# Optimization experiments

Hardware: AMD Instinct MI355X
Metric: run time of the kernel (lower is better)

## Reference

```python
import jax, jax.numpy as jnp
import numpy as np

NA = 100000   # author nodes
NP = 100000   # paper nodes
E = 500000    # edges per relation
H = 128       # hidden size
FA = 256      # author input features
FP = 128      # paper input features
LA = 4        # author labels
LP = 7        # paper labels


def setup_inputs() -> dict:
    key = jax.random.key(0)
    ks = iter(jax.random.split(key, 48))
    def rn(shape, scale=0.05):
        return jax.random.normal(next(ks), shape, jnp.float32) * scale
    inp = {}
    inp['x_author'] = jax.random.normal(next(ks), (NA, FA), jnp.float32)
    inp['x_paper'] = jax.random.normal(next(ks), (NP, FP), jnp.float32)
    inp['edge_index_p2a'] = jax.random.randint(next(ks), (2, E), 0, 100000, jnp.int64)  # row0: paper src, row1: author dst
    inp['edge_index_a2p'] = jax.random.randint(next(ks), (2, E), 0, 100000, jnp.int64)  # row0: author src, row1: paper dst
    # layer 1 convs (per message type): lin_src, lin_dst, lin_update(2H->H)
    inp['w1_p2a_src'] = rn((FP, H)); inp['b1_p2a_src'] = rn((H,))
    inp['w1_p2a_dst'] = rn((FA, H)); inp['b1_p2a_dst'] = rn((H,))
    inp['w1_p2a_upd'] = rn((2 * H, H)); inp['b1_p2a_upd'] = rn((H,))
    inp['w1_a2p_src'] = rn((FA, H)); inp['b1_a2p_src'] = rn((H,))
    inp['w1_a2p_dst'] = rn((FP, H)); inp['b1_a2p_dst'] = rn((H,))
    inp['w1_a2p_upd'] = rn((2 * H, H)); inp['b1_a2p_upd'] = rn((H,))
    # layer 2 convs (all dims = H)
    inp['w2_p2a_src'] = rn((H, H)); inp['b2_p2a_src'] = rn((H,))
    inp['w2_p2a_dst'] = rn((H, H)); inp['b2_p2a_dst'] = rn((H,))
    inp['w2_p2a_upd'] = rn((2 * H, H)); inp['b2_p2a_upd'] = rn((H,))
    inp['w2_a2p_src'] = rn((H, H)); inp['b2_a2p_src'] = rn((H,))
    inp['w2_a2p_dst'] = rn((H, H)); inp['b2_a2p_dst'] = rn((H,))
    inp['w2_a2p_upd'] = rn((2 * H, H)); inp['b2_a2p_upd'] = rn((H,))
    # batchnorm affine params per node type per layer
    inp['g1_a'] = jnp.ones((H,), jnp.float32); inp['be1_a'] = jnp.zeros((H,), jnp.float32)
    inp['g1_p'] = jnp.ones((H,), jnp.float32); inp['be1_p'] = jnp.zeros((H,), jnp.float32)
    inp['g2_a'] = jnp.ones((H,), jnp.float32); inp['be2_a'] = jnp.zeros((H,), jnp.float32)
    inp['g2_p'] = jnp.ones((H,), jnp.float32); inp['be2_p'] = jnp.zeros((H,), jnp.float32)
    # post message-passing heads
    inp['w_post_a'] = rn((H, LA)); inp['b_post_a'] = rn((LA,))
    inp['w_post_p'] = rn((H, LP)); inp['b_post_p'] = rn((LP,))
    return inp


def _mean_agg(x_src, src, dst, n_dst):
    # gather source features along edges, mean-scatter to destination nodes
    msg = x_src[src]                                            # [E, F]
    s = jax.ops.segment_sum(msg, dst, num_segments=n_dst)       # [n_dst, F]
    cnt = jax.ops.segment_sum(jnp.ones((dst.shape[0],), msg.dtype), dst, num_segments=n_dst)
    return s / jnp.maximum(cnt, 1.0)[:, None]


def _conv(x_src, x_dst, src, dst, ws, bs, wd, bd, wu, bu):
    agg = _mean_agg(x_src, src, dst, x_dst.shape[0])
    h = jnp.concatenate([x_dst @ wd + bd, agg @ ws + bs], axis=-1)   # [n_dst, 2H]
    return h @ wu + bu


def _bn_lrelu(x, g, b):
    # BatchNorm1d(eps=1) in training mode (batch stats, biased var) then LeakyReLU(0.01)
    m = x.mean(axis=0)
    v = x.var(axis=0)
    y = g * (x - m) / jnp.sqrt(v + 1.0) + b
    return jnp.where(y >= 0, y, 0.01 * y)


def reference(x_author, x_paper, edge_index_p2a, edge_index_a2p,
              w1_p2a_src, b1_p2a_src, w1_p2a_dst, b1_p2a_dst, w1_p2a_upd, b1_p2a_upd,
              w1_a2p_src, b1_a2p_src, w1_a2p_dst, b1_a2p_dst, w1_a2p_upd, b1_a2p_upd,
              w2_p2a_src, b2_p2a_src, w2_p2a_dst, b2_p2a_dst, w2_p2a_upd, b2_p2a_upd,
              w2_a2p_src, b2_a2p_src, w2_a2p_dst, b2_a2p_dst, w2_a2p_upd, b2_a2p_upd,
              g1_a, be1_a, g1_p, be1_p, g2_a, be2_a, g2_p, be2_p,
              w_post_a, b_post_a, w_post_p, b_post_p):
    src_pa, dst_pa = edge_index_p2a[0], edge_index_p2a[1]
    src_ap, dst_ap = edge_index_a2p[0], edge_index_a2p[1]
    # layer 1: per-message-type conv -> per-node-type BN + LeakyReLU
    h_a = _conv(x_paper, x_author, src_pa, dst_pa, w1_p2a_src, b1_p2a_src, w1_p2a_dst, b1_p2a_dst, w1_p2a_upd, b1_p2a_upd)
    h_p = _conv(x_author, x_paper, src_ap, dst_ap, w1_a2p_src, b1_a2p_src, w1_a2p_dst, b1_a2p_dst, w1_a2p_upd, b1_a2p_upd)
    h_a = _bn_lrelu(h_a, g1_a, be1_a)
    h_p = _bn_lrelu(h_p, g1_p, be1_p)
    # layer 2
    h_a2 = _conv(h_p, h_a, src_pa, dst_pa, w2_p2a_src, b2_p2a_src, w2_p2a_dst, b2_p2a_dst, w2_p2a_upd, b2_p2a_upd)
    h_p2 = _conv(h_a, h_p, src_ap, dst_ap, w2_a2p_src, b2_a2p_src, w2_a2p_dst, b2_a2p_dst, w2_a2p_upd, b2_a2p_upd)
    h_a2 = _bn_lrelu(h_a2, g2_a, be2_a)
    h_p2 = _bn_lrelu(h_p2, g2_p, be2_p)
    # post message-passing heads per node type
    out_a = h_a2 @ w_post_a + b_post_a   # [NA, LA]
    out_p = h_p2 @ w_post_p + b_post_p   # [NP, LP]
    return (out_a, out_p)
```

## Files before the change

kernel.cpp:

```cpp
#include <hip/hip_runtime.h>

#define NN 100000
#define NE 500000
#define HD 128
#define NBLK 391

typedef float f32x4v __attribute__((ext_vector_type(4)));
typedef short s16x8  __attribute__((ext_vector_type(8)));

static __device__ __forceinline__ unsigned f2bf_bits(float f){
  unsigned u = __float_as_uint(f);
  return (u + 0x7FFF + ((u >> 16) & 1)) >> 16;
}
static __device__ __forceinline__ void split8v(f32x4v v0, f32x4v v1, s16x8& hi, s16x8& lo){
  #pragma unroll
  for (int j = 0; j < 4; ++j){
    float f = v0[j];
    unsigned hb = f2bf_bits(f);
    hi[j] = (short)hb; lo[j] = (short)f2bf_bits(f - __uint_as_float(hb << 16));
  }
  #pragma unroll
  for (int j = 0; j < 4; ++j){
    float f = v1[j];
    unsigned hb = f2bf_bits(f);
    hi[4+j] = (short)hb; lo[4+j] = (short)f2bf_bits(f - __uint_as_float(hb << 16));
  }
}

static __device__ __forceinline__ float4 bn_lrelu4(float4 v, float4 sc, float4 sh){
  v.x = v.x*sc.x + sh.x; v.x = v.x >= 0.f ? v.x : 0.01f*v.x;
  v.y = v.y*sc.y + sh.y; v.y = v.y >= 0.f ? v.y : 0.01f*v.y;
  v.z = v.z*sc.z + sh.z; v.z = v.z >= 0.f ? v.z : 0.01f*v.z;
  v.w = v.w*sc.w + sh.w; v.w = v.w >= 0.f ? v.w : 0.01f*v.w;
  return v;
}
static __device__ __forceinline__ f32x4v bn_lrelu4v(f32x4v v, f32x4v sc, f32x4v sh){
  #pragma unroll
  for (int j = 0; j < 4; ++j){
    float y = v[j]*sc[j] + sh[j];
    v[j] = y >= 0.f ? y : 0.01f*y;
  }
  return v;
}

__global__ void k_count(const int* __restrict__ ei_pa, const int* __restrict__ ei_ap,
                        int* __restrict__ deg2){
  int idx = blockIdx.x * 256 + threadIdx.x;
  if (idx < NE)        atomicAdd(&deg2[      ei_pa[NE + idx]], 1);
  else if (idx < 2*NE) atomicAdd(&deg2[NN + ei_ap[NE + (idx - NE)]], 1);
}

__global__ void k_bsum(const int* __restrict__ deg2, int* __restrict__ bsum){
  int rel = blockIdx.x / NBLK, b = blockIdx.x % NBLK;
  int i = b*256 + threadIdx.x;
  int v = (i < NN) ? deg2[rel*NN + i] : 0;
  __shared__ int s[256];
  s[threadIdx.x] = v; __syncthreads();
  for (int o = 128; o > 0; o >>= 1){
    if (threadIdx.x < o) s[threadIdx.x] += s[threadIdx.x + o];
    __syncthreads();
  }
  if (threadIdx.x == 0) bsum[rel*512 + b] = s[0];
}

__global__ void k_bscan(const int* __restrict__ bsum, int* __restrict__ bsoff){
  int rel = blockIdx.x, t = threadIdx.x;
  int v = (t < NBLK) ? bsum[rel*512 + t] : 0;
  __shared__ int s[512];
  s[t] = v; __syncthreads();
  for (int o = 1; o < 512; o <<= 1){
    int x = (t >= o) ? s[t - o] : 0;
    __syncthreads();
    s[t] += x;
    __syncthreads();
  }
  bsoff[rel*512 + t] = s[t] - v;
}

__global__ void k_scanC(const int* __restrict__ deg2, const int* __restrict__ bsoff,
                        int* __restrict__ off2, int* __restrict__ cur2){
  int rel = blockIdx.x / NBLK, b = blockIdx.x % NBLK;
  int i = b*256 + threadIdx.x, t = threadIdx.x;
  int v = (i < NN) ? deg2[rel*NN + i] : 0;
  __shared__ int s[256];
  s[t] = v; __syncthreads();
  for (int o = 1; o < 256; o <<= 1){
    int x = (t >= o) ? s[t - o] : 0;
    __syncthreads();
    s[t] += x;
    __syncthreads();
  }
  if (i < NN){
    int o = bsoff[rel*512 + b] + s[t] - v;
    off2[rel*NN + i] = o;
    cur2[rel*NN + i] = o;
  }
}

__global__ void k_fill(const int* __restrict__ ei_pa, const int* __restrict__ ei_ap,
                       int* __restrict__ cur2,
                       int* __restrict__ col_pa, int* __restrict__ col_ap){
  int idx = blockIdx.x * 256 + threadIdx.x;
  if (idx < NE){
    int s = ei_pa[idx], d = ei_pa[NE + idx];
    int pos = atomicAdd(&cur2[d], 1);
    col_pa[pos] = s;
  } else if (idx < 2*NE){
    int e = idx - NE;
    int s = ei_ap[e], d = ei_ap[NE + e];
    int pos = atomicAdd(&cur2[NN + d], 1);
    col_ap[pos] = s;
  }
}

struct FoldDesc { const float* A; const float* B; short* T; int off; };
struct FoldArgs { FoldDesc d[8]; int rs[9]; };

__global__ void k_fold(FoldArgs fa){
  int row = blockIdx.x;
  int seg = 0;
  #pragma unroll
  for (int s = 0; s < 8; ++s) if (row >= fa.rs[s+1]) seg = s + 1;
  int m = row - fa.rs[seg];
  const float* A = fa.d[seg].A + (size_t)m * 128;
  const float* B = fa.d[seg].B;
  int n = threadIdx.x;
  float acc = 0.f;
  for (int k = 0; k < 128; ++k) acc += A[k] * B[k*128 + n];
  unsigned hb = f2bf_bits(acc);
  float hf = __uint_as_float(hb << 16);
  unsigned lb = f2bf_bits(acc - hf);
  int gkc = fa.d[seg].off + (m >> 5), quad = (m >> 3) & 3, j = m & 7;
  int lane = quad*16 + (n & 15), nt = n >> 4;
  size_t fb = (size_t)((gkc*8 + nt)*2)*512 + lane*8 + j;
  fa.d[seg].T[fb]       = (short)hb;
  fa.d[seg].T[fb + 512] = (short)lb;
}

struct BiasArgs { const float* bd[4]; const float* bs[4]; const float* wu[4];
                  const float* bu[4]; float* outb[4]; };
__global__ void k_biasfold(BiasArgs ba){
  int s = blockIdx.x, j = threadIdx.x;
  const float* wu = ba.wu[s];
  float acc = ba.bu[s][j];
  for (int k = 0; k < 128; ++k)
    acc += ba.bd[s][k] * wu[k*128 + j] + ba.bs[s][k] * wu[(128 + k)*128 + j];
  ba.outb[s][j] = acc;
}

template<int DUALB, int GATHER, int BN>
__global__ __launch_bounds__(256)
void k_gemm3(const float* __restrict__ A1, int lda1, int KC1,
             const float* __restrict__ bn1,
             const float* __restrict__ A2, int lda2, int KC2,
             const short* __restrict__ BfA, const short* __restrict__ BfB,
             const float* __restrict__ bias,
             const int* __restrict__ goff, const int* __restrict__ gdeg,
             const int* __restrict__ gcol, const float* __restrict__ gsrc,
             float* __restrict__ C1, float* __restrict__ C2,
             float* __restrict__ stats, int M)
{
  constexpr int BUFSZ = DUALB ? 32768 : 16384;
  constexpr int LDSSZ = 2*BUFSZ + (BN ? 1024 : 0);
  __shared__ __align__(16) char smem[LDSSZ];
  float* bnlds = (float*)(smem + 2*BUFSZ);

  const int tid  = threadIdx.x;
  const int wave = tid >> 6, lane = tid & 63;
  const int li   = lane & 15, quad = lane >> 4;
  const int rowT = blockIdx.x * 128 + wave * 32;
  const int KCtot = KC1 + KC2;

  f32x4v acc1[2][8];
  f32x4v acc2[2][8];
  #pragma unroll
  for (int mt = 0; mt < 2; ++mt)
    #pragma unroll
    for (int nt = 0; nt < 8; ++nt){
      acc1[mt][nt] = (f32x4v){0.f, 0.f, 0.f, 0.f};
      if (DUALB) acc2[mt][nt] = (f32x4v){0.f, 0.f, 0.f, 0.f};
    }

  const float* b1[2];
  const float* b2[2];
  #pragma unroll
  for (int mt = 0; mt < 2; ++mt){
    int row = rowT + mt*16 + li;
    int r = (row < M) ? row : 0;
    b1[mt] = A1 + (size_t)r*lda1 + quad*8;
    b2[mt] = A2 ? (A2 + (size_t)r*lda2 + quad*8) : (const float*)nullptr;
  }

  auto loadA = [&](int gkc, f32x4v (&dst)[2][2]){
    #pragma unroll
    for (int mt = 0; mt < 2; ++mt){
      const float* p = (gkc < KC1) ? (b1[mt] + gkc*32) : (b2[mt] + (gkc - KC1)*32);
      dst[mt][0] = *(const f32x4v*)p;
      dst[mt][1] = *(const f32x4v*)(p + 4);
    }
  };

  auto stageB = [&](int kc, int bufIdx){
    char* d = smem + bufIdx * BUFSZ;
    const char* sA = (const char*)BfA + (size_t)kc * 16384;
    #pragma unroll
    for (int c = 0; c < 4; ++c){
      int off = c*4096 + wave*1024;
      __builtin_amdgcn_global_load_lds(
          (const __attribute__((address_space(1))) unsigned int*)(sA + off + lane*16),
          (__attribute__((address_space(3))) unsigned int*)(d + off),
          16, 0, 0);
    }
    if (DUALB && kc < KC1){
      const char* sB = (const char*)BfB + (size_t)kc * 16384;
      #pragma unroll
      for (int c = 0; c < 4; ++c){
        int off = c*4096 + wave*1024;
        __builtin_amdgcn_global_load_lds(
            (const __attribute__((address_space(1))) unsigned int*)(sB + off + lane*16),
            (__attribute__((address_space(3))) unsigned int*)(d + 16384 + off),
            16, 0, 0);
      }
    }
  };

  auto computeK = [&](int j, int bufIdx, f32x4v (&a)[2][2]){
    if (BN && j < KC1){
      int base = j*32 + quad*8;
      f32x4v sc0 = *(const f32x4v*)(bnlds + base);
      f32x4v sc1 = *(const f32x4v*)(bnlds + base + 4);
      f32x4v sh0 = *(const f32x4v*)(bnlds + base + 128);
      f32x4v sh1 = *(const f32x4v*)(bnlds + base + 132);
      #pragma unroll
      for (int mt = 0; mt < 2; ++mt){
        a[mt][0] = bn_lrelu4v(a[mt][0], sc0, sh0);
        a[mt][1] = bn_lrelu4v(a[mt][1], sc1, sh1);
      }
    }
    s16x8 ah[2], al[2];
    #pragma unroll
    for (int mt = 0; mt < 2; ++mt) split8v(a[mt][0], a[mt][1], ah[mt], al[mt]);

    const short* base = (const short*)(smem + bufIdx*BUFSZ) + lane*8;
    __builtin_amdgcn_s_setprio(1);
    #pragma unroll
    for (int nt = 0; nt < 8; ++nt){
      const short* bp = base + (nt << 10);
      s16x8 bh = *(const s16x8*)bp;
      s16x8 bl = *(const s16x8*)(bp + 512);
      #pragma unroll
      for (int mt = 0; mt < 2; ++mt){
        acc1[mt][nt] = __builtin_amdgcn_mfma_f32_16x16x32_bf16(ah[mt], bh, acc1[mt][nt], 0, 0, 0);
        acc1[mt][nt] = __builtin_amdgcn_mfma_f32_16x16x32_bf16(al[mt], bh, acc1[mt][nt], 0, 0, 0);
        acc1[mt][nt] = __builtin_amdgcn_mfma_f32_16x16x32_bf16(ah[mt], bl, acc1[mt][nt], 0, 0, 0);
      }
    }
    if (DUALB && j < KC1){
      const short* base2 = base + 8192;
      #pragma unroll
      for (int nt = 0; nt < 8; ++nt){
        const short* bp = base2 + (nt << 10);
        s16x8 bh = *(const s16x8*)bp;
        s16x8 bl = *(const s16x8*)(bp + 512);
        #pragma unroll
        for (int mt = 0; mt < 2; ++mt){
          acc2[mt][nt] = __builtin_amdgcn_mfma_f32_16x16x32_bf16(ah[mt], bh, acc2[mt][nt], 0, 0, 0);
          acc2[mt][nt] = __builtin_amdgcn_mfma_f32_16x16x32_bf16(al[mt], bh, acc2[mt][nt], 0, 0, 0);
          acc2[mt][nt] = __builtin_amdgcn_mfma_f32_16x16x32_bf16(ah[mt], bl, acc2[mt][nt], 0, 0, 0);
        }
      }
    }
    __builtin_amdgcn_s_setprio(0);
  };

  if (BN) bnlds[tid] = bn1[tid];
  f32x4v aC[2][2], aN1[2][2], aN2[2][2];
  stageB(0, 0);
  loadA(0, aC);
  loadA(1, aN1);
  if (BN) asm volatile("s_waitcnt lgkmcnt(0)" ::: "memory");

  for (int j = 0; j < KCtot; ++j){
    if (j + 1 < KCtot) asm volatile("s_waitcnt vmcnt(4)" ::: "memory");
    else               asm volatile("s_waitcnt vmcnt(0)" ::: "memory");
    __builtin_amdgcn_s_barrier();
    __builtin_amdgcn_sched_barrier(0);
    if (j + 1 < KCtot) stageB(j + 1, (j + 1) & 1);
    if (j + 2 < KCtot) loadA(j + 2, aN2);
    computeK(j, j & 1, aC);
    #pragma unroll
    for (int mt = 0; mt < 2; ++mt){
      aC[mt][0] = aN1[mt][0]; aC[mt][1] = aN1[mt][1];
      aN1[mt][0] = aN2[mt][0]; aN1[mt][1] = aN2[mt][1];
    }
  }

  __syncthreads();
  float* Cw = (float*)smem + wave*2048;
  int col4 = lane & 31;
  float4 s1 = make_float4(0.f,0.f,0.f,0.f), s2 = s1;

  auto epi_pass = [&](f32x4v (&ac)[2][8], float* Cout, const float* bptr,
                      bool wStats){
    float4 bias4 = make_float4(0.f,0.f,0.f,0.f);
    if (bptr) bias4 = ((const float4*)bptr)[col4];
    #pragma unroll
    for (int mt = 0; mt < 2; ++mt){
      #pragma unroll
      for (int r = 0; r < 4; ++r){
        int lr = quad*4 + r;
        #pragma unroll
        for (int nt = 0; nt < 8; ++nt){
          int c = nt*16 + li;
          int chunk = ((c >> 2) + 2*quad) & 31;
          Cw[lr*128 + chunk*4 + (c & 3)] = ac[mt][nt][r];
        }
      }
      #pragma unroll
      for (int i = 0; i < 8; ++i){
        int lr = i*2 + (lane >> 5);
        int grow = rowT + mt*16 + lr;
        if (grow >= M) continue;
        int chunk = (col4 + 2*(lr >> 2)) & 31;
        float4 v = *(const float4*)(Cw + lr*128 + chunk*4);
        v.x += bias4.x; v.y += bias4.y; v.z += bias4.z; v.w += bias4.w;
        if (GATHER && wStats){
          int cnt = gdeg[grow], s0g = goff[grow];
          float4 g = make_float4(0.f,0.f,0.f,0.f);
          for (int e = 0; e < cnt; ++e){
            int src = gcol[s0g + e];
            float4 gv = ((const float4*)(gsrc + ((size_t)src << 7)))[col4];
            g.x += gv.x; g.y += gv.y; g.z += gv.z; g.w += gv.w;
          }
          float inv = 1.0f / (float)(cnt > 0 ? cnt : 1);
          v.x += g.x*inv; v.y += g.y*inv; v.z += g.z*inv; v.w += g.w*inv;
        }
        ((float4*)(Cout + ((size_t)grow << 7)))[col4] = v;
        if (wStats){
          s1.x += v.x; s1.y += v.y; s1.z += v.z; s1.w += v.w;
          s2.x += v.x*v.x; s2.y += v.y*v.y; s2.z += v.z*v.z; s2.w += v.w*v.w;
        }
      }
    }
  };

  epi_pass(acc1, C1, bias, stats != nullptr);
  if (DUALB) epi_pass(acc2, C2, nullptr, false);

  if (stats){
    __syncthreads();
    float* Ss = (float*)smem;
    ((float4*)Ss)[tid*2]     = s1;
    ((float4*)Ss)[tid*2 + 1] = s2;
    __syncthreads();
    int c = tid & 127, kind = tid >> 7;
    int cc4 = c >> 2, comp = c & 3;
    float s = 0.f;
    #pragma unroll
    for (int wv = 0; wv < 4; ++wv)
      #pragma unroll
      for (int hf = 0; hf < 2; ++hf)
        s += Ss[(wv*64 + hf*32 + cc4)*8 + kind*4 + comp];
    atomicAdd(&stats[kind*128 + c], s);
  }
}

__global__ __launch_bounds__(256)
void k_agg(const float* __restrict__ t, const int* __restrict__ off,
           const int* __restrict__ deg, const int* __restrict__ col,
           float* __restrict__ o, const float* __restrict__ bn){
  int slot = threadIdx.x >> 5, col4 = threadIdx.x & 31;
  int d = blockIdx.x*8 + slot;
  if (d >= NN) return;
  float4 sc4, sh4;
  bool hasbn = (bn != nullptr);
  if (hasbn){ sc4 = ((const float4*)bn)[col4]; sh4 = ((const float4*)(bn+128))[col4]; }
  int s0 = off[d], cnt = deg[d];
  float4 a0 = make_float4(0.f,0.f,0.f,0.f), a1 = a0;
  int i = 0;
  for (; i + 4 <= cnt; i += 4){
    int sa = col[s0+i], sb = col[s0+i+1], sct = col[s0+i+2], sd = col[s0+i+3];
    float4 v0 = ((const float4*)(t + ((size_t)sa << 7)))[col4];
    float4 v1 = ((const float4*)(t + ((size_t)sb << 7)))[col4];
    float4 v2 = ((const float4*)(t + ((size_t)sct << 7)))[col4];
    float4 v3 = ((const float4*)(t + ((size_t)sd << 7)))[col4];
    if (hasbn){
      v0 = bn_lrelu4(v0, sc4, sh4); v1 = bn_lrelu4(v1, sc4, sh4);
      v2 = bn_lrelu4(v2, sc4, sh4); v3 = bn_lrelu4(v3, sc4, sh4);
    }
    a0.x += v0.x + v2.x; a0.y += v0.y + v2.y; a0.z += v0.z + v2.z; a0.w += v0.w + v2.w;
    a1.x += v1.x + v3.x; a1.y += v1.y + v3.y; a1.z += v1.z + v3.z; a1.w += v1.w + v3.w;
  }
  for (; i < cnt; ++i){
    int sa = col[s0+i];
    float4 v0 = ((const float4*)(t + ((size_t)sa << 7)))[col4];
    if (hasbn) v0 = bn_lrelu4(v0, sc4, sh4);
    a0.x += v0.x; a0.y += v0.y; a0.z += v0.z; a0.w += v0.w;
  }
  float inv = 1.0f / (float)(cnt > 0 ? cnt : 1);
  float4 r;
  r.x = (a0.x + a1.x)*inv; r.y = (a0.y + a1.y)*inv;
  r.z = (a0.z + a1.z)*inv; r.w = (a0.w + a1.w)*inv;
  ((float4*)(o + ((size_t)d << 7)))[col4] = r;
}

__global__ void k_bnprep(const float* __restrict__ stats, const float* __restrict__ g,
                         const float* __restrict__ b, float* __restrict__ sc, int M){
  int c = threadIdx.x;
  float invN = 1.0f / (float)M;
  float m  = stats[c] * invN;
  float var = stats[128 + c] * invN - m*m;
  float scale = g[c] / sqrtf(var + 1.0f);
  sc[c] = scale;
  sc[128 + c] = b[c] - m*scale;
}

template<int LC>
__global__ void k_head(const float* __restrict__ h, const float* __restrict__ bn,
                       const float* __restrict__ w, const float* __restrict__ b,
                       float* __restrict__ o, int M){
  __shared__ float ws[128*LC];
  __shared__ float bs[LC];
  __shared__ float bsc[256];
  for (int i = threadIdx.x; i < 128*LC; i += 256) ws[i] = w[i];
  if (threadIdx.x < LC) bs[threadIdx.x] = b[threadIdx.x];
  if (threadIdx.x < 256) bsc[threadIdx.x] = bn[threadIdx.x];
  __syncthreads();
  int r = blockIdx.x*256 + threadIdx.x;
  if (r >= M) return;
  float acc[LC];
  #pragma unroll
  for (int c = 0; c < LC; ++c) acc[c] = bs[c];
  const float4* hr = (const float4*)(h + ((size_t)r << 7));
  for (int k4 = 0; k4 < 32; ++k4){
    float4 v = hr[k4];
    float4 sc = ((const float4*)bsc)[k4];
    float4 sh = ((const float4*)bsc)[32 + k4];
    v = bn_lrelu4(v, sc, sh);
    int k = k4*4;
    #pragma unroll
    for (int c = 0; c < LC; ++c)
      acc[c] += v.x*ws[k*LC+c] + v.y*ws[(k+1)*LC+c] + v.z*ws[(k+2)*LC+c] + v.w*ws[(k+3)*LC+c];
  }
  #pragma unroll
  for (int c = 0; c < LC; ++c) o[(size_t)r*LC + c] = acc[c];
}

extern "C" void kernel_launch(void* const* d_in, const int* in_sizes, int n_in,
                              void* d_out, int out_size, void* d_ws, size_t ws_size,
                              hipStream_t stream) {
  const float* x_author = (const float*)d_in[0];
  const float* x_paper  = (const float*)d_in[1];
  const int*   ei_pa    = (const int*)d_in[2];
  const int*   ei_ap    = (const int*)d_in[3];

  char* p = (char*)d_ws;
  auto alloc = [&](size_t bytes) -> void* {
    void* r = (void*)p; p += (bytes + 255) & ~(size_t)255; return r;
  };
  short* T_l1a  = (short*)alloc(12u*16384);
  short* T_l1ps = (short*)alloc( 8u*16384);
  short* T_l1pd = (short*)alloc( 4u*16384);
  short* T_l2a  = (short*)alloc( 8u*16384);
  short* T_l2p  = (short*)alloc( 8u*16384);
  float* w1a_b = (float*)alloc(128*4);      float* w1p_b = (float*)alloc(128*4);
  float* w2a_b = (float*)alloc(128*4);      float* w2p_b = (float*)alloc(128*4);
  float* stats4 = (float*)alloc(4*256*4);
  float* bnsc4  = (float*)alloc(4*256*4);
  int* deg2  = (int*)alloc(2*NN*4);
  int* off2  = (int*)alloc(2*NN*4);
  int* cur2  = (int*)alloc(2*NN*4);
  int* col_pa = (int*)alloc(NE*4);
  int* col_ap = (int*)alloc(NE*4);
  int* bsum  = (int*)alloc(1024*4);
  int* bsoff = (int*)alloc(1024*4);
  const size_t NB = (size_t)NN * 128;
  float* B1 = (float*)alloc(NB*4);
  float* B2 = (float*)alloc(NB*4);
  float* B3 = (float*)alloc(NB*4);
  float* B4 = (float*)alloc(NB*4);

  hipMemsetAsync(deg2, 0, 2*NN*4, stream);
  hipMemsetAsync(stats4, 0, 4*256*4, stream);
  k_count<<<(2*NE + 255)/256, 256, 0, stream>>>(ei_pa, ei_ap, deg2);
  k_bsum <<<2*NBLK, 256, 0, stream>>>(deg2, bsum);
  k_bscan<<<2, 512, 0, stream>>>(bsum, bsoff);
  k_scanC<<<2*NBLK, 256, 0, stream>>>(deg2, bsoff, off2, cur2);
  k_fill <<<(2*NE + 255)/256, 256, 0, stream>>>(ei_pa, ei_ap, cur2, col_pa, col_ap);

  FoldArgs fa;
  const float* wu1a = (const float*)d_in[8];
  const float* wu1p = (const float*)d_in[14];
  const float* wu2a = (const float*)d_in[20];
  const float* wu2p = (const float*)d_in[26];
  fa.d[0] = { (const float*)d_in[6],  wu1a,           T_l1a,  0 };
  fa.d[1] = { (const float*)d_in[4],  wu1a + 128*128, T_l1a,  8 };
  fa.d[2] = { (const float*)d_in[10], wu1p + 128*128, T_l1ps, 0 };
  fa.d[3] = { (const float*)d_in[12], wu1p,           T_l1pd, 0 };
  fa.d[4] = { (const float*)d_in[18], wu2a,           T_l2a,  0 };
  fa.d[5] = { (const float*)d_in[16], wu2a + 128*128, T_l2a,  4 };
  fa.d[6] = { (const float*)d_in[24], wu2p,           T_l2p,  0 };
  fa.d[7] = { (const float*)d_in[22], wu2p + 128*128, T_l2p,  4 };
  int rows[8] = {256,128,256,128,128,128,128,128};
  fa.rs[0] = 0;
  for (int i = 0; i < 8; ++i) fa.rs[i+1] = fa.rs[i] + rows[i];
  k_fold<<<fa.rs[8], 128, 0, stream>>>(fa);

  BiasArgs ba;
  ba.bd[0]=(const float*)d_in[7];  ba.bs[0]=(const float*)d_in[5];  ba.wu[0]=wu1a; ba.bu[0]=(const float*)d_in[9];  ba.outb[0]=w1a_b;
  ba.bd[1]=(const float*)d_in[13]; ba.bs[1]=(const float*)d_in[11]; ba.wu[1]=wu1p; ba.bu[1]=(const float*)d_in[15]; ba.outb[1]=w1p_b;
  ba.bd[2]=(const float*)d_in[19]; ba.bs[2]=(const float*)d_in[17]; ba.wu[2]=wu2a; ba.bu[2]=(const float*)d_in[21]; ba.outb[2]=w2a_b;
  ba.bd[3]=(const float*)d_in[25]; ba.bs[3]=(const float*)d_in[23]; ba.wu[3]=wu2p; ba.bu[3]=(const float*)d_in[27]; ba.outb[3]=w2p_b;
  k_biasfold<<<4, 128, 0, stream>>>(ba);

  const int GG = (NN + 127)/128;
  const int AGG_GRID = (NN + 7)/8;
  const int* off_pa = off2;        const int* deg_pa = deg2;
  const int* off_ap = off2 + NN;   const int* deg_ap = deg2 + NN;
  float* st_a1 = stats4;       float* st_p1 = stats4 + 256;
  float* st_a2 = stats4 + 512; float* st_p2 = stats4 + 768;
  float* sc_a1 = bnsc4;        float* sc_p1 = bnsc4 + 256;
  float* sc_a2 = bnsc4 + 512;  float* sc_p2 = bnsc4 + 768;

  k_agg<<<AGG_GRID, 256, 0, stream>>>(x_paper, off_pa, deg_pa, col_pa, B4, nullptr);
  k_gemm3<1,0,0><<<GG, 256, 0, stream>>>(
      x_author, 256, 8, nullptr, B4, 128, 4, T_l1a, T_l1ps, w1a_b,
      nullptr, nullptr, nullptr, nullptr, B1, B3, st_a1, NN);
  k_bnprep<<<1, 128, 0, stream>>>(st_a1, (const float*)d_in[28], (const float*)d_in[29], sc_a1, NN);

  k_gemm3<0,1,0><<<GG, 256, 0, stream>>>(
      x_paper, 128, 4, nullptr, nullptr, 128, 0, T_l1pd, nullptr, w1p_b,
      off_ap, deg_ap, col_ap, B3, B2, nullptr, st_p1, NN);
  k_bnprep<<<1, 128, 0, stream>>>(st_p1, (const float*)d_in[30], (const float*)d_in[31], sc_p1, NN);

  k_agg<<<AGG_GRID, 256, 0, stream>>>(B2, off_pa, deg_pa, col_pa, B4, sc_p1);
  k_gemm3<0,0,1><<<GG, 256, 0, stream>>>(
      B1, 128, 4, sc_a1, B4, 128, 4, T_l2a, nullptr, w2a_b,
      nullptr, nullptr, nullptr, nullptr, B3, nullptr, st_a2, NN);
  k_bnprep<<<1, 128, 0, stream>>>(st_a2, (const float*)d_in[32], (const float*)d_in[33], sc_a2, NN);
  k_head<4><<<(NN + 255)/256, 256, 0, stream>>>(B3, sc_a2, (const float*)d_in[36],
                                                (const float*)d_in[37], (float*)d_out, NN);

  k_agg<<<AGG_GRID, 256, 0, stream>>>(B1, off_ap, deg_ap, col_ap, B4, sc_a1);
  k_gemm3<0,0,1><<<GG, 256, 0, stream>>>(
      B2, 128, 4, sc_p1, B4, 128, 4, T_l2p, nullptr, w2p_b,
      nullptr, nullptr, nullptr, nullptr, B1, nullptr, st_p2, NN);
  k_bnprep<<<1, 128, 0, stream>>>(st_p2, (const float*)d_in[34], (const float*)d_in[35], sc_p2, NN);
  k_head<7><<<(NN + 255)/256, 256, 0, stream>>>(B1, sc_p2, (const float*)d_in[38],
                                                (const float*)d_in[39], (float*)d_out + (size_t)NN*4, NN);
}
```

Baseline: 944.6 us.

## Store intermediate activations as 16-bit fixed-point and restructure GEMM staging

All intermediate node-feature buffers change from fp32 to int16 fixed-point with scale 2048, halving the bytes moved by the gather/aggregation and GEMM kernels. The fused gather in the layer-1 paper GEMM epilogue is split out into a separate k_agg pass whose result feeds the GEMM as an extra addend. The GEMM's double-buffered B staging is replaced by single-buffer staging with a barrier before and after each stage. Fixed-point quantization with clamping adds rounding error and saturates values beyond ±16, and the removed double buffering may expose load latency.

```diff
diff --git a/kernel.cpp b/kernel.cpp
--- a/kernel.cpp
+++ b/kernel.cpp
@@ -7,6 +7,28 @@
 
 typedef float f32x4v __attribute__((ext_vector_type(4)));
 typedef short s16x8  __attribute__((ext_vector_type(8)));
+
+#define QS 2048.0f
+#define IQS (1.0f/2048.0f)
+
+static __device__ __forceinline__ short enc1(float v){
+  float x = v * QS;
+  x = fminf(32767.f, fmaxf(-32767.f, x));
+  return (short)__float2int_rn(x);
+}
+static __device__ __forceinline__ short4 enc4(float4 v){
+  short4 s; s.x = enc1(v.x); s.y = enc1(v.y); s.z = enc1(v.z); s.w = enc1(v.w);
+  return s;
+}
+static __device__ __forceinline__ float4 dec4(short4 q){
+  return make_float4(q.x*IQS, q.y*IQS, q.z*IQS, q.w*IQS);
+}
+static __device__ __forceinline__ void dec8v(s16x8 q, f32x4v& v0, f32x4v& v1){
+  #pragma unroll
+  for (int j = 0; j < 4; ++j) v0[j] = (float)q[j] * IQS;
+  #pragma unroll
+  for (int j = 0; j < 4; ++j) v1[j] = (float)q[4+j] * IQS;
+}
 
 static __device__ __forceinline__ unsigned f2bf_bits(float f){
   unsigned u = __float_as_uint(f);
@@ -148,22 +170,19 @@
   ba.outb[s][j] = acc;
 }
 
-template<int DUALB, int GATHER, int BN>
+template<int A1Q, int DUALB, int BN>
 __global__ __launch_bounds__(256)
-void k_gemm3(const float* __restrict__ A1, int lda1, int KC1,
+void k_gemm4(const void* __restrict__ A1v, int lda1, int KC1,
              const float* __restrict__ bn1,
-             const float* __restrict__ A2, int lda2, int KC2,
+             const short* __restrict__ A2, int lda2, int KC2,
              const short* __restrict__ BfA, const short* __restrict__ BfB,
-             const float* __restrict__ bias,
-             const int* __restrict__ goff, const int* __restrict__ gdeg,
-             const int* __restrict__ gcol, const float* __restrict__ gsrc,
-             float* __restrict__ C1, float* __restrict__ C2,
+             const float* __restrict__ bias, const short* __restrict__ extra,
+             short* __restrict__ C, short* __restrict__ C2,
              float* __restrict__ stats, int M)
 {
-  constexpr int BUFSZ = DUALB ? 32768 : 16384;
-  constexpr int LDSSZ = 2*BUFSZ + (BN ? 1024 : 0);
+  constexpr int LDSSZ = 32768 + (BN ? 1024 : 0);
   __shared__ __align__(16) char smem[LDSSZ];
-  float* bnlds = (float*)(smem + 2*BUFSZ);
+  float* bnlds = (float*)(smem + 32768);
 
   const int tid  = threadIdx.x;
   const int wave = tid >> 6, lane = tid & 63;
@@ -181,67 +200,92 @@
       if (DUALB) acc2[mt][nt] = (f32x4v){0.f, 0.f, 0.f, 0.f};
     }
 
-  const float* b1[2];
-  const float* b2[2];
+  const void*  b1[2];
+  const short* b2[2];
   #pragma unroll
   for (int mt = 0; mt < 2; ++mt){
     int row = rowT + mt*16 + li;
     int r = (row < M) ? row : 0;
-    b1[mt] = A1 + (size_t)r*lda1 + quad*8;
-    b2[mt] = A2 ? (A2 + (size_t)r*lda2 + quad*8) : (const float*)nullptr;
+    if (A1Q) b1[mt] = (const void*)((const short*)A1v + (size_t)r*lda1 + quad*8);
+    else     b1[mt] = (const void*)((const float*)A1v + (size_t)r*lda1 + quad*8);
+    b2[mt] = A2 ? (A2 + (size_t)r*lda2 + quad*8) : (const short*)nullptr;
   }
 
   auto loadA = [&](int gkc, f32x4v (&dst)[2][2]){
     #pragma unroll
     for (int mt = 0; mt < 2; ++mt){
-      const float* p = (gkc < KC1) ? (b1[mt] + gkc*32) : (b2[mt] + (gkc - KC1)*32);
-      dst[mt][0] = *(const f32x4v*)p;
-      dst[mt][1] = *(const f32x4v*)(p + 4);
+      if (gkc < KC1){
+        if (A1Q){
+          const short* p = (const short*)b1[mt] + gkc*32;
+          dst[mt][0] = *(const f32x4v*)p;
+        } else {
+          const float* p = (const float*)b1[mt] + gkc*32;
+          dst[mt][0] = *(const f32x4v*)p;
+          dst[mt][1] = *(const f32x4v*)(p + 4);
+        }
+      } else {
+        const short* p = b2[mt] + (gkc - KC1)*32;
+        dst[mt][0] = *(const f32x4v*)p;
+      }
     }
   };
 
-  auto stageB = [&](int kc, int bufIdx){
-    char* d = smem + bufIdx * BUFSZ;
-    const char* sA = (const char*)BfA + (size_t)kc * 16384;
-    #pragma unroll
-    for (int c = 0; c < 4; ++c){
-      int off = c*4096 + wave*1024;
-      __builtin_amdgcn_global_load_lds(
-          (const __attribute__((address_space(1))) unsigned int*)(sA + off + lane*16),
-          (__attribute__((address_space(3))) unsigned int*)(d + off),
-          16, 0, 0);
-    }
-    if (DUALB && kc < KC1){
-      const char* sB = (const char*)BfB + (size_t)kc * 16384;
+  auto stage = [&](int g){
+    if (!DUALB){
+      const char* s = (const char*)BfA + (size_t)g * 16384;
+      #pragma unroll
+      for (int c = 0; c < 8; ++c){
+        int off = c*4096 + wave*1024;
+        __builtin_amdgcn_global_load_lds(
+            (const __attribute__((address_space(1))) unsigned int*)(s + off + lane*16),
+            (__attribute__((address_space(3))) unsigned int*)(smem + off),
+            16, 0, 0);
+      }
+    } else {
+      const char* sA = (const char*)BfA + (size_t)g * 16384;
       #pragma unroll
       for (int c = 0; c < 4; ++c){
         int off = c*4096 + wave*1024;
         __builtin_amdgcn_global_load_lds(
-            (const __attribute__((address_space(1))) unsigned int*)(sB + off + lane*16),
-            (__attribute__((address_space(3))) unsigned int*)(d + 16384 + off),
+            (const __attribute__((address_space(1))) unsigned int*)(sA + off + lane*16),
+            (__attribute__((address_space(3))) unsigned int*)(smem + off),
             16, 0, 0);
       }
+      if (g < KC1){
+        const char* sB = (const char*)BfB + (size_t)g * 16384;
+        #pragma unroll
+        for (int c = 0; c < 4; ++c){
+          int off = c*4096 + wave*1024;
+          __builtin_amdgcn_global_load_lds(
+              (const __attribute__((address_space(1))) unsigned int*)(sB + off + lane*16),
+              (__attribute__((address_space(3))) unsigned int*)(smem + 16384 + off),
+              16, 0, 0);
+        }
+      }
     }
   };
 
-  auto computeK = [&](int j, int bufIdx, f32x4v (&a)[2][2]){
-    if (BN && j < KC1){
-      int base = j*32 + quad*8;
-      f32x4v sc0 = *(const f32x4v*)(bnlds + base);
-      f32x4v sc1 = *(const f32x4v*)(bnlds + base + 4);
-      f32x4v sh0 = *(const f32x4v*)(bnlds + base + 128);
-      f32x4v sh1 = *(const f32x4v*)(bnlds + base + 132);
-      #pragma unroll
-      for (int mt = 0; mt < 2; ++mt){
-        a[mt][0] = bn_lrelu4v(a[mt][0], sc0, sh0);
-        a[mt][1] = bn_lrelu4v(a[mt][1], sc1, sh1);
-      }
-    }
+  auto computeK = [&](int gkc, const short* base, f32x4v (&raw)[2][2]){
     s16x8 ah[2], al[2];
     #pragma unroll
-    for (int mt = 0; mt < 2; ++mt) split8v(a[mt][0], a[mt][1], ah[mt], al[mt]);
-
-    const short* base = (const short*)(smem + bufIdx*BUFSZ) + lane*8;
+    for (int mt = 0; mt < 2; ++mt){
+      f32x4v v0, v1;
+      if (A1Q || gkc >= KC1){
+        dec8v(__builtin_bit_cast(s16x8, raw[mt][0]), v0, v1);
+      } else {
+        v0 = raw[mt][0]; v1 = raw[mt][1];
+      }
+      if (BN && gkc < KC1){
+        int bb = gkc*32 + quad*8;
+        f32x4v sc0 = *(const f32x4v*)(bnlds + bb);
+        f32x4v sc1 = *(const f32x4v*)(bnlds + bb + 4);
+        f32x4v sh0 = *(const f32x4v*)(bnlds + bb + 128);
+        f32x4v sh1 = *(const f32x4v*)(bnlds + bb + 132);
+        v0 = bn_lrelu4v(v0, sc0, sh0);
+        v1 = bn_lrelu4v(v1, sc1, sh1);
+      }
+      split8v(v0, v1, ah[mt], al[mt]);
+    }
     __builtin_amdgcn_s_setprio(1);
     #pragma unroll
     for (int nt = 0; nt < 8; ++nt){
@@ -255,7 +299,7 @@
         acc1[mt][nt] = __builtin_amdgcn_mfma_f32_16x16x32_bf16(ah[mt], bl, acc1[mt][nt], 0, 0, 0);
       }
     }
-    if (DUALB && j < KC1){
+    if (DUALB && gkc < KC1){
       const short* base2 = base + 8192;
       #pragma unroll
       for (int nt = 0; nt < 8; ++nt){
@@ -273,25 +317,25 @@
     __builtin_amdgcn_s_setprio(0);
   };
 
-  if (BN) bnlds[tid] = bn1[tid];
-  f32x4v aC[2][2], aN1[2][2], aN2[2][2];
-  stageB(0, 0);
-  loadA(0, aC);
-  loadA(1, aN1);
-  if (BN) asm volatile("s_waitcnt lgkmcnt(0)" ::: "memory");
-
-  for (int j = 0; j < KCtot; ++j){
-    if (j + 1 < KCtot) asm volatile("s_waitcnt vmcnt(4)" ::: "memory");
-    else               asm volatile("s_waitcnt vmcnt(0)" ::: "memory");
-    __builtin_amdgcn_s_barrier();
-    __builtin_amdgcn_sched_barrier(0);
-    if (j + 1 < KCtot) stageB(j + 1, (j + 1) & 1);
-    if (j + 2 < KCtot) loadA(j + 2, aN2);
-    computeK(j, j & 1, aC);
-    #pragma unroll
-    for (int mt = 0; mt < 2; ++mt){
-      aC[mt][0] = aN1[mt][0]; aC[mt][1] = aN1[mt][1];
-      aN1[mt][0] = aN2[mt][0]; aN1[mt][1] = aN2[mt][1];
+  if (BN && tid < 256) bnlds[tid] = bn1[tid];
+  f32x4v cur[2][2], nxt[2][2];
+  loadA(0, cur);
+
+  const int KCG = DUALB ? 1 : 2;
+  for (int g = 0; g < KCtot; g += KCG){
+    if (g) __syncthreads();
+    stage(g);
+    __syncthreads();
+    #pragma unroll
+    for (int kk = 0; kk < (DUALB ? 1 : 2); ++kk){
+      int gkc = g + kk;
+      if (gkc + 1 < KCtot) loadA(gkc + 1, nxt);
+      const short* base = (const short*)smem + (DUALB ? 0 : kk*8192) + lane*8;
+      computeK(gkc, base, cur);
+      #pragma unroll
+      for (int mt = 0; mt < 2; ++mt){
+        cur[mt][0] = nxt[mt][0]; cur[mt][1] = nxt[mt][1];
+      }
     }
   }
 
@@ -300,7 +344,7 @@
   int col4 = lane & 31;
   float4 s1 = make_float4(0.f,0.f,0.f,0.f), s2 = s1;
 
-  auto epi_pass = [&](f32x4v (&ac)[2][8], float* Cout, const float* bptr,
+  auto epi_pass = [&](f32x4v (&ac)[2][8], short* Cout, const float* bptr,
                       bool wStats){
     float4 bias4 = make_float4(0.f,0.f,0.f,0.f);
     if (bptr) bias4 = ((const float4*)bptr)[col4];
@@ -324,18 +368,12 @@
         int chunk = (col4 + 2*(lr >> 2)) & 31;
         float4 v = *(const float4*)(Cw + lr*128 + chunk*4);
         v.x += bias4.x; v.y += bias4.y; v.z += bias4.z; v.w += bias4.w;
-        if (GATHER && wStats){
-          int cnt = gdeg[grow], s0g = goff[grow];
-          float4 g = make_float4(0.f,0.f,0.f,0.f);
-          for (int e = 0; e < cnt; ++e){
-            int src = gcol[s0g + e];
-            float4 gv = ((const float4*)(gsrc + ((size_t)src << 7)))[col4];
-            g.x += gv.x; g.y += gv.y; g.z += gv.z; g.w += gv.w;
-          }
-          float inv = 1.0f / (float)(cnt > 0 ? cnt : 1);
-          v.x += g.x*inv; v.y += g.y*inv; v.z += g.z*inv; v.w += g.w*inv;
+        if (extra && wStats){
+          short4 q = *(const short4*)(extra + ((size_t)grow << 7) + col4*4);
+          float4 e = dec4(q);
+          v.x += e.x; v.y += e.y; v.z += e.z; v.w += e.w;
         }
-        ((float4*)(Cout + ((size_t)grow << 7)))[col4] = v;
+        *(short4*)(Cout + ((size_t)grow << 7) + col4*4) = enc4(v);
         if (wStats){
           s1.x += v.x; s1.y += v.y; s1.z += v.z; s1.w += v.w;
           s2.x += v.x*v.x; s2.y += v.y*v.y; s2.z += v.z*v.z; s2.w += v.w*v.w;
@@ -344,7 +382,7 @@
     }
   };
 
-  epi_pass(acc1, C1, bias, stats != nullptr);
+  epi_pass(acc1, C, bias, true);
   if (DUALB) epi_pass(acc2, C2, nullptr, false);
 
   if (stats){
@@ -365,43 +403,47 @@
   }
 }
 
+template<int IS>
 __global__ __launch_bounds__(256)
-void k_agg(const float* __restrict__ t, const int* __restrict__ off,
+void k_agg(const void* __restrict__ tv, const int* __restrict__ off,
            const int* __restrict__ deg, const int* __restrict__ col,
-           float* __restrict__ o, const float* __restrict__ bn){
+           short* __restrict__ o, const float* __restrict__ bn){
+  const float* tf = (const float*)tv;
+  const short* ts = (const short*)tv;
   int slot = threadIdx.x >> 5, col4 = threadIdx.x & 31;
   int d = blockIdx.x*8 + slot;
   if (d >= NN) return;
   float4 sc4, sh4;
-  bool hasbn = (bn != nullptr);
+  bool hasbn = IS && (bn != nullptr);
   if (hasbn){ sc4 = ((const float4*)bn)[col4]; sh4 = ((const float4*)(bn+128))[col4]; }
+  auto loadrow = [&](int row) -> float4 {
+    float4 v;
+    if (IS) v = dec4(*(const short4*)(ts + ((size_t)row << 7) + col4*4));
+    else    v = ((const float4*)(tf + ((size_t)row << 7)))[col4];
+    if (hasbn) v = bn_lrelu4(v, sc4, sh4);
+    return v;
+  };
   int s0 = off[d], cnt = deg[d];
   float4 a0 = make_float4(0.f,0.f,0.f,0.f), a1 = a0;
   int i = 0;
   for (; i + 4 <= cnt; i += 4){
     int sa = col[s0+i], sb = col[s0+i+1], sct = col[s0+i+2], sd = col[s0+i+3];
-    float4 v0 = ((const float4*)(t + ((size_t)sa << 7)))[col4];
-    float4 v1 = ((const float4*)(t + ((size_t)sb << 7)))[col4];
-    float4 v2 = ((const float4*)(t + ((size_t)sct << 7)))[col4];
-    float4 v3 = ((const float4*)(t + ((size_t)sd << 7)))[col4];
-    if (hasbn){
-      v0 = bn_lrelu4(v0, sc4, sh4); v1 = bn_lrelu4(v1, sc4, sh4);
-      v2 = bn_lrelu4(v2, sc4, sh4); v3 = bn_lrelu4(v3, sc4, sh4);
-    }
+    float4 v0 = loadrow(sa);
+    float4 v1 = loadrow(sb);
+    float4 v2 = loadrow(sct);
+    float4 v3 = loadrow(sd);
     a0.x += v0.x + v2.x; a0.y += v0.y + v2.y; a0.z += v0.z + v2.z; a0.w += v0.w + v2.w;
     a1.x += v1.x + v3.x; a1.y += v1.y + v3.y; a1.z += v1.z + v3.z; a1.w += v1.w + v3.w;
   }
   for (; i < cnt; ++i){
-    int sa = col[s0+i];
-    float4 v0 = ((const float4*)(t + ((size_t)sa << 7)))[col4];
-    if (hasbn) v0 = bn_lrelu4(v0, sc4, sh4);
+    float4 v0 = loadrow(col[s0+i]);
     a0.x += v0.x; a0.y += v0.y; a0.z += v0.z; a0.w += v0.w;
   }
   float inv = 1.0f / (float)(cnt > 0 ? cnt : 1);
   float4 r;
   r.x = (a0.x + a1.x)*inv; r.y = (a0.y + a1.y)*inv;
   r.z = (a0.z + a1.z)*inv; r.w = (a0.w + a1.w)*inv;
-  ((float4*)(o + ((size_t)d << 7)))[col4] = r;
+  *(short4*)(o + ((size_t)d << 7) + col4*4) = enc4(r);
 }
 
 __global__ void k_bnprep(const float* __restrict__ stats, const float* __restrict__ g,
@@ -416,7 +458,7 @@
 }
 
 template<int LC>
-__global__ void k_head(const float* __restrict__ h, const float* __restrict__ bn,
+__global__ void k_head(const short* __restrict__ h, const float* __restrict__ bn,
                        const float* __restrict__ w, const float* __restrict__ b,
                        float* __restrict__ o, int M){
   __shared__ float ws[128*LC];
@@ -431,9 +473,9 @@
   float acc[LC];
   #pragma unroll
   for (int c = 0; c < LC; ++c) acc[c] = bs[c];
-  const float4* hr = (const float4*)(h + ((size_t)r << 7));
+  const short* hr = h + ((size_t)r << 7);
   for (int k4 = 0; k4 < 32; ++k4){
-    float4 v = hr[k4];
+    float4 v = dec4(((const short4*)hr)[k4]);
     float4 sc = ((const float4*)bsc)[k4];
     float4 sh = ((const float4*)bsc)[32 + k4];
     v = bn_lrelu4(v, sc, sh);
@@ -475,10 +517,10 @@
   int* bsum  = (int*)alloc(1024*4);
   int* bsoff = (int*)alloc(1024*4);
   const size_t NB = (size_t)NN * 128;
-  float* B1 = (float*)alloc(NB*4);
-  float* B2 = (float*)alloc(NB*4);
-  float* B3 = (float*)alloc(NB*4);
-  float* B4 = (float*)alloc(NB*4);
+  short* B1 = (short*)alloc(NB*2);
+  short* B2 = (short*)alloc(NB*2);
+  short* B3 = (short*)alloc(NB*2);
+  short* B4 = (short*)alloc(NB*2);
 
   hipMemsetAsync(deg2, 0, 2*NN*4, stream);
   hipMemsetAsync(stats4, 0, 4*256*4, stream);
@@ -522,29 +564,30 @@
   float* sc_a1 = bnsc4;        float* sc_p1 = bnsc4 + 256;
   float* sc_a2 = bnsc4 + 512;  float* sc_p2 = bnsc4 + 768;
 
-  k_agg<<<AGG_GRID, 256, 0, stream>>>(x_paper, off_pa, deg_pa, col_pa, B4, nullptr);
-  k_gemm3<1,0,0><<<GG, 256, 0, stream>>>(
+  k_agg<0><<<AGG_GRID, 256, 0, stream>>>(x_paper, off_pa, deg_pa, col_pa, B4, nullptr);
+  k_gemm4<0,1,0><<<GG, 256, 0, stream>>>(
       x_author, 256, 8, nullptr, B4, 128, 4, T_l1a, T_l1ps, w1a_b,
-      nullptr, nullptr, nullptr, nullptr, B1, B3, st_a1, NN);
+      nullptr, B1, B3, st_a1, NN);
   k_bnprep<<<1, 128, 0, stream>>>(st_a1, (const float*)d_in[28], (const float*)d_in[29], sc_a1, NN);
 
-  k_gemm3<0,1,0><<<GG, 256, 0, stream>>>(
-      x_paper, 128, 4, nullptr, nullptr, 128, 0, T_l1pd, nullptr, w1p_b,
-      off_ap, deg_ap, col_ap, B3, B2, nullptr, st_p1, NN);
+  k_agg<1><<<AGG_GRID, 256, 0, stream>>>(B3, off_ap, deg_ap, col_ap, B4, nullptr);
+  k_gemm4<0,0,0><<<GG, 256, 0, stream>>>(
+      x_paper, 128, 4, nullptr, nullptr, 0, 0, T_l1pd, nullptr, w1p_b,
+      B4, B2, nullptr, st_p1, NN);
   k_bnprep<<<1, 128, 0, stream>>>(st_p1, (const float*)d_in[30], (const float*)d_in[31], sc_p1, NN);
 
-  k_agg<<<AGG_GRID, 256, 0, stream>>>(B2, off_pa, deg_pa, col_pa, B4, sc_p1);
-  k_gemm3<0,0,1><<<GG, 256, 0, stream>>>(
+  k_agg<1><<<AGG_GRID, 256, 0, stream>>>(B2, off_pa, deg_pa, col_pa, B4, sc_p1);
+  k_gemm4<1,0,1><<<GG, 256, 0, stream>>>(
       B1, 128, 4, sc_a1, B4, 128, 4, T_l2a, nullptr, w2a_b,
-      nullptr, nullptr, nullptr, nullptr, B3, nullptr, st_a2, NN);
+      nullptr, B3, nullptr, st_a2, NN);
   k_bnprep<<<1, 128, 0, stream>>>(st_a2, (const float*)d_in[32], (const float*)d_in[33], sc_a2, NN);
   k_head<4><<<(NN + 255)/256, 256, 0, stream>>>(B3, sc_a2, (const float*)d_in[36],
                                                 (const float*)d_in[37], (float*)d_out, NN);
 
-  k_agg<<<AGG_GRID, 256, 0, stream>>>(B1, off_ap, deg_ap, col_ap, B4, sc_a1);
-  k_gemm3<0,0,1><<<GG, 256, 0, stream>>>(
+  k_agg<1><<<AGG_GRID, 256, 0, stream>>>(B1, off_ap, deg_ap, col_ap, B4, sc_a1);
+  k_gemm4<1,0,1><<<GG, 256, 0, stream>>>(
       B2, 128, 4, sc_p1, B4, 128, 4, T_l2p, nullptr, w2p_b,
-      nullptr, nullptr, nullptr, nullptr, B1, nullptr, st_p2, NN);
+      nullptr, B1, nullptr, st_p2, NN);
   k_bnprep<<<1, 128, 0, stream>>>(st_p2, (const float*)d_in[34], (const float*)d_in[35], sc_p2, NN);
   k_head<7><<<(NN + 255)/256, 256, 0, stream>>>(B1, sc_p2, (const float*)d_in[38],
                                                 (const float*)d_in[39], (float*)d_out + (size_t)NN*4, NN);
```

New measurement: 884.4 us. 6.4% less time.
